# Kernel optimization log

Measured on AMD Instinct MI355X. Metric: run time of the kernel, lower is better.

Reference implementation:

```python
import jax, jax.numpy as jnp
import numpy as np
from functools import partial

B, N = 4, 4096
WIDTH, HEADS, HD = 768, 12, 64
MINI, CONV_W = 16, 4
TTT_BASE_LR = 1.0
THETA = 10000.0
EPS = 1e-6


def _rope_table():
    half = HD // 2
    freqs = 1.0 / THETA ** (np.arange(0, HD, 2)[:half].astype(np.float32) / HD)
    t = np.arange(2 * MINI)
    f = np.outer(t, freqs).astype(np.float32)
    return jnp.asarray(np.cos(f)), jnp.asarray(np.sin(f))

_COS, _SIN = _rope_table()


def apply_rope(x, cos, sin):
    # x: [B,N,H,HD]; cos/sin: [N, HD//2]; pairs are (x[2i], x[2i+1])
    xe, xo = x[..., 0::2], x[..., 1::2]
    c, s = cos[None, :, None, :], sin[None, :, None, :]
    return jnp.stack([xe * c - xo * s, xe * s + xo * c], axis=-1).reshape(x.shape)


def ln_fwd(x, g, b):
    mu = x.mean(-1, keepdims=True)
    std = jnp.sqrt(x.var(-1, keepdims=True) + EPS)
    return g * ((x - mu) / std) + b


def ln_fused_l2_bwd(x, target, g, b):
    # grad of 0.5*||LN(x)-target||^2 w.r.t. x (official TTT fused form)
    D = x.shape[-1]
    mu = x.mean(-1, keepdims=True)
    std = jnp.sqrt(x.var(-1, keepdims=True) + EPS)
    x_hat = (x - mu) / std
    gxh = ((g * x_hat + b) - target) * g
    return (D * gxh - gxh.sum(-1, keepdims=True)
            - x_hat * (gxh * x_hat).sum(-1, keepdims=True)) / (D * std)


def causal_dwconv(x, kernel, bias):
    # depthwise causal conv: x [B,N,C], kernel [W,1,C], left-pad W-1
    y = jax.lax.conv_general_dilated(
        x, kernel, (1,), [(CONV_W - 1, 0)],
        dimension_numbers=('NWC', 'WIO', 'NWC'), feature_group_count=WIDTH)
    return y + bias


def _mini_step(ln_g, ln_b, carry, inp):
    W1, b1h = carry
    XQ, XK, XV, eta = inp  # [m,hd] x3, eta [m,m]
    Z1 = XK @ W1 + b1h
    grad = ln_fused_l2_bwd(Z1, XV - XK, ln_g, ln_b)
    Attn = jnp.tril(XQ @ XK.T)
    b1_bar = b1h - jnp.tril(eta) @ grad
    Z1_bar = XQ @ W1 - (eta * Attn) @ grad + b1_bar
    last_eta = eta[-1][:, None]
    W1_new = W1 - (last_eta * XK).T @ grad
    b1_new = b1h - jnp.sum(last_eta * grad, axis=0, keepdims=True)
    out = XQ + ln_fwd(Z1_bar, ln_g, ln_b)
    return (W1_new, b1_new), out


def ttt_forward(hidden_states, wq, wv, wo, wg,
                conv_q_kernel, conv_q_bias, conv_k_kernel, conv_k_bias,
                W1, b1, ttt_norm_scale, ttt_norm_bias,
                lr_kernel, lr_bias, learnable_token_idx,
                post_norm_scale, post_norm_bias):
    Bsz, Nlen, _ = hidden_states.shape
    xqk = hidden_states @ wq
    XV = hidden_states @ wv
    XQ = causal_dwconv(xqk, conv_q_kernel, conv_q_bias)
    XK = causal_dwconv(xqk, conv_k_kernel, conv_k_bias)
    XQ = XQ.reshape(Bsz, Nlen, HEADS, HD)
    XK = XK.reshape(Bsz, Nlen, HEADS, HD)
    XV = XV.reshape(Bsz, Nlen, HEADS, HD)

    pos = jnp.arange(Nlen) % MINI  # RoPE restarts each mini-batch (official)
    XQ = apply_rope(XQ, _COS[pos], _SIN[pos])
    XK = apply_rope(XK, _COS[pos], _SIN[pos])

    def to_mb(x):  # [B,N,H,hd] -> [B,H,n_mini,mini,hd]
        return x.reshape(Bsz, -1, MINI, HEADS, HD).transpose(0, 3, 1, 2, 4)
    XQ, XK, XV = to_mb(XQ), to_mb(XK), to_mb(XV)

    # learnable per-head, per-token learning rate -> eta [B,H,n_mini,mini,mini]
    X_mb = hidden_states.reshape(Bsz, -1, MINI, WIDTH)
    ttt_lr = jax.nn.sigmoid(jnp.einsum('bnmw,hw->bhnm', X_mb, lr_kernel[..., 0])
                            + lr_bias[None, :, None, :])
    ttt_lr = TTT_BASE_LR * ttt_lr / HD
    token_idx = jnp.maximum(1.0 / jnp.arange(1, MINI + 1, dtype=jnp.float32)
                            + learnable_token_idx, 0.0)
    eta = token_idx[None, None, None, :, None] * ttt_lr[:, :, :, None, :]

    def per_head(xq, xk, xv, e, w1, b1h, g, bln):
        step = partial(_mini_step, g, bln)
        _, out = jax.lax.scan(step, (w1, b1h), (xq, xk, xv, e))
        return out.reshape(-1, HD)  # [N, hd]

    per_batch = jax.vmap(per_head, in_axes=(0, 0, 0, 0, 0, 0, 0, 0))
    out = jax.vmap(per_batch, in_axes=(0, 0, 0, 0, None, None, None, None))(
        XQ, XK, XV, eta, W1, b1, ttt_norm_scale, ttt_norm_bias)  # [B,H,N,hd]
    out = out.transpose(0, 2, 1, 3).reshape(Bsz, Nlen, WIDTH)

    z = ln_fwd(out, post_norm_scale, post_norm_bias)  # post_norm
    gate = jax.nn.gelu(hidden_states @ wg)            # GLU gating
    return (gate * z) @ wo


def setup_inputs() -> dict:
    key = jax.random.key(0)
    ks = jax.random.split(key, 12)
    std = 0.02
    f32 = jnp.float32
    return {
        'hidden_states': jax.random.normal(ks[0], (B, N, WIDTH), f32),
        'wq': jax.random.normal(ks[1], (WIDTH, HEADS * HD), f32) * std,
        'wv': jax.random.normal(ks[2], (WIDTH, HEADS * HD), f32) * std,
        'wo': jax.random.normal(ks[3], (WIDTH, WIDTH), f32) * std,
        'wg': jax.random.normal(ks[4], (WIDTH, WIDTH), f32) * std,
        'conv_q_kernel': jax.random.normal(ks[5], (CONV_W, 1, WIDTH), f32) * 0.5,
        'conv_q_bias': jnp.zeros((WIDTH,), f32),
        'conv_k_kernel': jax.random.normal(ks[6], (CONV_W, 1, WIDTH), f32) * 0.5,
        'conv_k_bias': jnp.zeros((WIDTH,), f32),
        'W1': jax.random.normal(ks[7], (HEADS, HD, HD), f32) * std,
        'b1': jnp.zeros((HEADS, 1, HD), f32),
        'ttt_norm_scale': jnp.ones((HEADS, HD), f32),
        'ttt_norm_bias': jnp.zeros((HEADS, HD), f32),
        'lr_kernel': jax.random.normal(ks[8], (HEADS, WIDTH, 1), f32) * std,
        'lr_bias': jnp.zeros((HEADS, 1), f32),
        'learnable_token_idx': jax.random.normal(ks[9], (MINI,), f32) * 0.01,
        'post_norm_scale': jnp.ones((WIDTH,), f32),
        'post_norm_bias': jnp.zeros((WIDTH,), f32),
    }


def reference(hidden_states, wq, wv, wo, wg, conv_q_kernel, conv_q_bias,
              conv_k_kernel, conv_k_bias, W1, b1, ttt_norm_scale, ttt_norm_bias,
              lr_kernel, lr_bias, learnable_token_idx, post_norm_scale, post_norm_bias):
    return ttt_forward(hidden_states, wq, wv, wo, wg, conv_q_kernel, conv_q_bias,
                       conv_k_kernel, conv_k_bias, W1, b1, ttt_norm_scale,
                       ttt_norm_bias, lr_kernel, lr_bias, learnable_token_idx,
                       post_norm_scale, post_norm_bias)
```

## Files before the change

### kernel.cpp

```cpp
#include <hip/hip_runtime.h>
#include <math.h>

#define WIDTH 768
#define HEADS 12
#define HD 64
#define MINI 16
#define NSEQ 4096
#define BATCH 4
#define NMB (NSEQ/MINI)
#define EPS 1e-6f

typedef __attribute__((ext_vector_type(8))) short bf16x8;
typedef __attribute__((ext_vector_type(4))) float f32x4;
typedef __attribute__((ext_vector_type(4))) int   i32x4;

__device__ __forceinline__ float bfu2f(unsigned short h) {
    return __uint_as_float(((unsigned)h) << 16);
}
__device__ __forceinline__ void tsplit(float f, unsigned short& h, unsigned short& l) {
    unsigned uh = __float_as_uint(f) & 0xffff0000u;
    h = (unsigned short)(uh >> 16);
    l = (unsigned short)(__float_as_uint(f - __uint_as_float(uh)) >> 16);
}
__device__ __forceinline__ unsigned tpack(float f) {
    unsigned uh = __float_as_uint(f) & 0xffff0000u;
    return uh | (__float_as_uint(f - __uint_as_float(uh)) >> 16);
}
__device__ __forceinline__ void barrier_lgkm() {
    asm volatile("s_waitcnt lgkmcnt(0)\n\ts_barrier" ::: "memory");
}

__global__ __launch_bounds__(256)
void hsplit_kernel(const float* __restrict__ in, unsigned short* __restrict__ hi,
                   unsigned short* __restrict__ lo)
{
    size_t idx = ((size_t)blockIdx.x * 256 + threadIdx.x) * 4;
    float4 v = *(const float4*)(in + idx);
    ushort4 h, l;
    tsplit(v.x, h.x, l.x); tsplit(v.y, h.y, l.y);
    tsplit(v.z, h.z, l.z); tsplit(v.w, h.w, l.w);
    *(ushort4*)(hi + idx) = h;
    *(ushort4*)(lo + idx) = l;
}

__global__ __launch_bounds__(256)
void wtconv_kernel(const float* __restrict__ w, unsigned short* __restrict__ hiT,
                   unsigned short* __restrict__ loT)
{
    __shared__ float sT[64][65];
    int k0 = blockIdx.y * 64, n0 = blockIdx.x * 64;
    int t = threadIdx.x, r = t >> 2, cs = (t & 3) * 16;
#pragma unroll
    for (int i = 0; i < 16; i += 4)
        *(float4*)&sT[r][cs + i] = *(const float4*)&w[(size_t)(k0 + r) * WIDTH + n0 + cs + i];
    __syncthreads();
    ushort4 hb[4], lb[4];
#pragma unroll
    for (int i = 0; i < 16; i++) {
        unsigned short hh, ll;
        tsplit(sT[cs + i][r], hh, ll);
        ((unsigned short*)hb)[i] = hh;
        ((unsigned short*)lb)[i] = ll;
    }
#pragma unroll
    for (int i = 0; i < 4; i++) {
        *(ushort4*)&hiT[(size_t)(n0 + r) * WIDTH + k0 + cs + i * 4] = hb[i];
        *(ushort4*)&loT[(size_t)(n0 + r) * WIDTH + k0 + cs + i * 4] = lb[i];
    }
}

template<int ACT>
__global__ __launch_bounds__(256, 2)
void gemm_bf3(const unsigned short* __restrict__ Ah, const unsigned short* __restrict__ Al,
              const unsigned short* __restrict__ BhT, const unsigned short* __restrict__ BlT,
              float* __restrict__ C, int M, int N, int K)
{
    __shared__ unsigned short sAh[128 * 40], sAl[128 * 40];
    __shared__ unsigned short sBh[128 * 40], sBl[128 * 40];
    const int tid = threadIdx.x;
    const int bm = blockIdx.y * 128, bn = blockIdx.x * 128;
    const int w = tid >> 6, lane = tid & 63, quad = lane >> 4, m16 = lane & 15;
    const int mw = (w & 1) * 64, nw = (w >> 1) * 64;
    const int srow = tid >> 1, sseg = (tid & 1) * 16;
    f32x4 acc[4][4];
#pragma unroll
    for (int a = 0; a < 4; a++)
#pragma unroll
        for (int c = 0; c < 4; c++) acc[a][c] = (f32x4){0.f, 0.f, 0.f, 0.f};

    for (int k0 = 0; k0 < K; k0 += 32) {
        uint4 va0 = *(const uint4*)(Ah + (size_t)(bm + srow) * K + k0 + sseg);
        uint4 va1 = *(const uint4*)(Ah + (size_t)(bm + srow) * K + k0 + sseg + 8);
        uint4 vb0 = *(const uint4*)(Al + (size_t)(bm + srow) * K + k0 + sseg);
        uint4 vb1 = *(const uint4*)(Al + (size_t)(bm + srow) * K + k0 + sseg + 8);
        uint4 vc0 = *(const uint4*)(BhT + (size_t)(bn + srow) * K + k0 + sseg);
        uint4 vc1 = *(const uint4*)(BhT + (size_t)(bn + srow) * K + k0 + sseg + 8);
        uint4 vd0 = *(const uint4*)(BlT + (size_t)(bn + srow) * K + k0 + sseg);
        uint4 vd1 = *(const uint4*)(BlT + (size_t)(bn + srow) * K + k0 + sseg + 8);
        __syncthreads();
        *(uint4*)&sAh[srow * 40 + sseg] = va0; *(uint4*)&sAh[srow * 40 + sseg + 8] = va1;
        *(uint4*)&sAl[srow * 40 + sseg] = vb0; *(uint4*)&sAl[srow * 40 + sseg + 8] = vb1;
        *(uint4*)&sBh[srow * 40 + sseg] = vc0; *(uint4*)&sBh[srow * 40 + sseg + 8] = vc1;
        *(uint4*)&sBl[srow * 40 + sseg] = vd0; *(uint4*)&sBl[srow * 40 + sseg + 8] = vd1;
        __syncthreads();
        bf16x8 ah[4], al[4];
#pragma unroll
        for (int mt = 0; mt < 4; mt++) {
            ah[mt] = *(const bf16x8*)&sAh[(mw + mt * 16 + m16) * 40 + quad * 8];
            al[mt] = *(const bf16x8*)&sAl[(mw + mt * 16 + m16) * 40 + quad * 8];
        }
#pragma unroll
        for (int nt = 0; nt < 4; nt++) {
            bf16x8 bh8 = *(const bf16x8*)&sBh[(nw + nt * 16 + m16) * 40 + quad * 8];
            bf16x8 bl8 = *(const bf16x8*)&sBl[(nw + nt * 16 + m16) * 40 + quad * 8];
#pragma unroll
            for (int mt = 0; mt < 4; mt++) {
                acc[mt][nt] = __builtin_amdgcn_mfma_f32_16x16x32_bf16(ah[mt], bh8, acc[mt][nt], 0, 0, 0);
                acc[mt][nt] = __builtin_amdgcn_mfma_f32_16x16x32_bf16(al[mt], bh8, acc[mt][nt], 0, 0, 0);
                acc[mt][nt] = __builtin_amdgcn_mfma_f32_16x16x32_bf16(ah[mt], bl8, acc[mt][nt], 0, 0, 0);
            }
        }
    }
#pragma unroll
    for (int mt = 0; mt < 4; mt++)
#pragma unroll
        for (int nt = 0; nt < 4; nt++)
#pragma unroll
            for (int r = 0; r < 4; r++) {
                float v = acc[mt][nt][r];
                if (ACT == 1) {
                    float inner = 0.7978845608028654f * (v + 0.044715f * v * v * v);
                    v = 0.5f * v * (1.0f + tanhf(inner));
                }
                C[(size_t)(bm + mw + mt * 16 + quad * 4 + r) * N + bn + nw + nt * 16 + m16] = v;
            }
}

__global__ __launch_bounds__(384)
void conv_rope_kernel(const float* __restrict__ xqk,
                      const float* __restrict__ kq, const float* __restrict__ bq,
                      const float* __restrict__ kk, const float* __restrict__ bk,
                      unsigned short* __restrict__ XQh, unsigned short* __restrict__ XQl,
                      unsigned short* __restrict__ XKh, unsigned short* __restrict__ XKl)
{
    int bid = blockIdx.x;
    int n = bid & (NSEQ - 1);
    int b = bid >> 12;
    int p = threadIdx.x;
    int c = p * 2;
    int pp = p & 31;
    float qe = bq[c], qo = bq[c + 1], ke = bk[c], ko = bk[c + 1];
#pragma unroll
    for (int w = 0; w < 4; w++) {
        int nn = n - 3 + w;
        if (nn >= 0) {
            const float* xr = xqk + ((size_t)(bid - n + nn)) * WIDTH + c;
            float xe = xr[0], xo = xr[1];
            qe = fmaf(xe, kq[w * WIDTH + c], qe);
            qo = fmaf(xo, kq[w * WIDTH + c + 1], qo);
            ke = fmaf(xe, kk[w * WIDTH + c], ke);
            ko = fmaf(xo, kk[w * WIDTH + c + 1], ko);
        }
    }
    int pos = n & (MINI - 1);
    float freq = expf(-(float)pp * (9.210340371976184f / 32.0f));
    float ang = (float)pos * freq;
    float c_ = cosf(ang), s_ = sinf(ang);
    int hh = p >> 5;
    int cc = pp * 2;
    size_t o = ((size_t)(b * HEADS + hh) * NSEQ + n) * 64 + cc;
    float q0 = qe * c_ - qo * s_, q1 = qe * s_ + qo * c_;
    float k0 = ke * c_ - ko * s_, k1 = ke * s_ + ko * c_;
    ushort2 h2, l2;
    tsplit(q0, h2.x, l2.x); tsplit(q1, h2.y, l2.y);
    *(ushort2*)&XQh[o] = h2; *(ushort2*)&XQl[o] = l2;
    tsplit(k0, h2.x, l2.x); tsplit(k1, h2.y, l2.y);
    *(ushort2*)&XKh[o] = h2; *(ushort2*)&XKl[o] = l2;
}

__global__ __launch_bounds__(256)
void lr_kernel(const float* __restrict__ hidden, const float* __restrict__ lrk,
               const float* __restrict__ lrb, float* __restrict__ lr_buf)
{
    int wave = threadIdx.x >> 6;
    int lane = threadIdx.x & 63;
    int row = blockIdx.x * 4 + wave;
    int b = row >> 12;
    int n = row & (NSEQ - 1);
    const float* hr = hidden + (size_t)row * WIDTH;
    float hv[12];
#pragma unroll
    for (int t = 0; t < 12; t++) hv[t] = hr[lane + 64 * t];
    for (int h = 0; h < HEADS; h++) {
        const float* lk = lrk + h * WIDTH;
        float acc = 0.f;
#pragma unroll
        for (int t = 0; t < 12; t++) acc = fmaf(hv[t], lk[lane + 64 * t], acc);
#pragma unroll
        for (int m = 1; m < 64; m <<= 1) acc += __shfl_xor(acc, m);
        if (lane == 0) {
            float s = 1.0f / (1.0f + __expf(-(acc + lrb[h])));
            lr_buf[((size_t)(b * HEADS + h)) * NSEQ + n] = s * (1.0f / HD);
        }
    }
}

__global__ __launch_bounds__(256)
void scan3_kernel(const unsigned short* __restrict__ XQh, const unsigned short* __restrict__ XQl,
                  const unsigned short* __restrict__ XKh, const unsigned short* __restrict__ XKl,
                  const float* __restrict__ XVb, const float* __restrict__ lr_buf,
                  const float* __restrict__ W1g, const float* __restrict__ b1g,
                  const float* __restrict__ gln, const float* __restrict__ blnv,
                  const float* __restrict__ lti, float* __restrict__ out)
{
    __shared__ unsigned sXKp[16 * 68];
    __shared__ unsigned sGE[16 * 68];
    __shared__ unsigned sCB[16 * 20];
    __shared__ float    sU[64 * 68];
    __shared__ float    sRed1[16 * 12], sRed2[16 * 12], sRed3[16 * 12];
    __shared__ float    sB1d[64];

    const int tid = threadIdx.x;
    const int w = tid >> 6, lane = tid & 63;
    const int quad = lane >> 4, m16 = lane & 15;
    const int bh = blockIdx.x, b = bh / HEADS, h = bh - b * HEADS;
    const int jc = 16 * w + m16;
    const int j4 = 16 * w + quad * 4;

    float g4[4], b4[4], b1v[4];
#pragma unroll
    for (int r = 0; r < 4; r++) {
        g4[r] = gln[h * 64 + j4 + r];
        b4[r] = blnv[h * 64 + j4 + r];
        b1v[r] = b1g[h * 64 + j4 + r];
    }
    const float tok15 = fmaxf(1.0f / 16.0f + lti[15], 0.0f);
    float tki[4];
#pragma unroll
    for (int r = 0; r < 4; r++)
        tki[r] = fmaxf(1.0f / (float)(quad * 4 + r + 1) + lti[quad * 4 + r], 0.0f) / tok15;

    float W1f[2][8]; bf16x8 w1h[2], w1l[2];
#pragma unroll
    for (int kt = 0; kt < 2; kt++)
#pragma unroll
        for (int e = 0; e < 8; e++) {
            float f = W1g[h * 4096 + (kt * 32 + quad * 8 + e) * 64 + jc];
            W1f[kt][e] = f;
            unsigned short hh, ll; tsplit(f, hh, ll);
            w1h[kt][e] = (short)hh; w1l[kt][e] = (short)ll;
        }

    const unsigned short* xqh = XQh + (size_t)bh * NSEQ * 64;
    const unsigned short* xql = XQl + (size_t)bh * NSEQ * 64;
    const unsigned short* xkh = XKh + (size_t)bh * NSEQ * 64;
    const unsigned short* xkl = XKl + (size_t)bh * NSEQ * 64;
    const float* xvB = XVb + (size_t)b * NSEQ * WIDTH + h * 64;
    const float* lrB = lr_buf + (size_t)bh * NSEQ;
    float* outB = out + (size_t)b * NSEQ * WIDTH + h * 64;

    bf16x8 ones8;
#pragma unroll
    for (int e = 0; e < 8; e++) ones8[e] = (short)0x3F80;
    const bf16x8 zf = {0, 0, 0, 0, 0, 0, 0, 0};

    bf16x8 pqh[2], pql[2], pkh[2], pkl[2];
    float4 pxv; ushort4 pth, ptl, poh, pol; float plr;
    {
        const size_t tok = m16;
#pragma unroll
        for (int kt = 0; kt < 2; kt++) {
            pqh[kt] = *(const bf16x8*)(xqh + tok * 64 + kt * 32 + quad * 8);
            pql[kt] = *(const bf16x8*)(xql + tok * 64 + kt * 32 + quad * 8);
            pkh[kt] = *(const bf16x8*)(xkh + tok * 64 + kt * 32 + quad * 8);
            pkl[kt] = *(const bf16x8*)(xkl + tok * 64 + kt * 32 + quad * 8);
        }
        pxv = *(const float4*)(xvB + tok * WIDTH + j4);
        pth = *(const ushort4*)(xkh + tok * 64 + j4);
        ptl = *(const ushort4*)(xkl + tok * 64 + j4);
        poh = *(const ushort4*)(xqh + tok * 64 + j4);
        pol = *(const ushort4*)(xql + tok * 64 + j4);
        plr = lrB[m16];
    }

    for (int s = 0; s < NMB; s++) {
        bf16x8 qh[2] = {pqh[0], pqh[1]}, ql[2] = {pql[0], pql[1]};
        bf16x8 kh[2] = {pkh[0], pkh[1]}, kl[2] = {pkl[0], pkl[1]};
        float xv4[4] = {pxv.x, pxv.y, pxv.z, pxv.w};
        float xkt4[4], xqo4[4];
        xkt4[0] = bfu2f(pth.x) + bfu2f(ptl.x); xkt4[1] = bfu2f(pth.y) + bfu2f(ptl.y);
        xkt4[2] = bfu2f(pth.z) + bfu2f(ptl.z); xkt4[3] = bfu2f(pth.w) + bfu2f(ptl.w);
        xqo4[0] = bfu2f(poh.x) + bfu2f(pol.x); xqo4[1] = bfu2f(poh.y) + bfu2f(pol.y);
        xqo4[2] = bfu2f(poh.z) + bfu2f(pol.z); xqo4[3] = bfu2f(poh.w) + bfu2f(pol.w);
        const float lrc = plr;
        const float sc = tok15 * lrc;

#pragma unroll
        for (int kt = 0; kt < 2; kt++) {
            i32x4 p0, p1;
#pragma unroll
            for (int e = 0; e < 4; e++)
                p0[e] = (int)((((unsigned)(unsigned short)kh[kt][e]) << 16) | (unsigned short)kl[kt][e]);
#pragma unroll
            for (int e = 0; e < 4; e++)
                p1[e] = (int)((((unsigned)(unsigned short)kh[kt][4 + e]) << 16) | (unsigned short)kl[kt][4 + e]);
            *(i32x4*)&sXKp[m16 * 68 + kt * 32 + quad * 8] = p0;
            *(i32x4*)&sXKp[m16 * 68 + kt * 32 + quad * 8 + 4] = p1;
        }

        {
            const int sn = (s + 1 < NMB) ? s + 1 : s;
            const size_t tok = (size_t)sn * 16 + m16;
#pragma unroll
            for (int kt = 0; kt < 2; kt++) {
                pqh[kt] = *(const bf16x8*)(xqh + tok * 64 + kt * 32 + quad * 8);
                pql[kt] = *(const bf16x8*)(xql + tok * 64 + kt * 32 + quad * 8);
                pkh[kt] = *(const bf16x8*)(xkh + tok * 64 + kt * 32 + quad * 8);
                pkl[kt] = *(const bf16x8*)(xkl + tok * 64 + kt * 32 + quad * 8);
            }
            pxv = *(const float4*)(xvB + tok * WIDTH + j4);
            pth = *(const ushort4*)(xkh + tok * 64 + j4);
            ptl = *(const ushort4*)(xkl + tok * 64 + j4);
            poh = *(const ushort4*)(xqh + tok * 64 + j4);
            pol = *(const ushort4*)(xql + tok * 64 + j4);
            plr = lrB[(size_t)sn * 16 + m16];
        }

        f32x4 z1 = {0.f, 0.f, 0.f, 0.f}, zq = {0.f, 0.f, 0.f, 0.f};
#pragma unroll
        for (int kt = 0; kt < 2; kt++) {
            z1 = __builtin_amdgcn_mfma_f32_16x16x32_bf16(w1h[kt], kh[kt], z1, 0, 0, 0);
            z1 = __builtin_amdgcn_mfma_f32_16x16x32_bf16(w1h[kt], kl[kt], z1, 0, 0, 0);
            z1 = __builtin_amdgcn_mfma_f32_16x16x32_bf16(w1l[kt], kh[kt], z1, 0, 0, 0);
            zq = __builtin_amdgcn_mfma_f32_16x16x32_bf16(w1h[kt], qh[kt], zq, 0, 0, 0);
            zq = __builtin_amdgcn_mfma_f32_16x16x32_bf16(w1h[kt], ql[kt], zq, 0, 0, 0);
            zq = __builtin_amdgcn_mfma_f32_16x16x32_bf16(w1l[kt], qh[kt], zq, 0, 0, 0);
        }
        f32x4 at = {0.f, 0.f, 0.f, 0.f};
        if (w == 0) {
#pragma unroll
            for (int kt = 0; kt < 2; kt++) {
                at = __builtin_amdgcn_mfma_f32_16x16x32_bf16(qh[kt], kh[kt], at, 0, 0, 0);
                at = __builtin_amdgcn_mfma_f32_16x16x32_bf16(qh[kt], kl[kt], at, 0, 0, 0);
                at = __builtin_amdgcn_mfma_f32_16x16x32_bf16(ql[kt], kh[kt], at, 0, 0, 0);
            }
        }
#pragma unroll
        for (int r = 0; r < 4; r++) z1[r] += b1v[r];

        float s1p = (z1[0] + z1[1]) + (z1[2] + z1[3]);
        float s2p = (z1[0] * z1[0] + z1[1] * z1[1]) + (z1[2] * z1[2] + z1[3] * z1[3]);
        s1p += __shfl_xor(s1p, 16); s2p += __shfl_xor(s2p, 16);
        s1p += __shfl_xor(s1p, 32); s2p += __shfl_xor(s2p, 32);
        if (quad == 0) *(float2*)&sRed1[m16 * 12 + 2 * w] = make_float2(s1p, s2p);
        if (w == 0) {
            i32x4 cw;
#pragma unroll
            for (int r = 0; r < 4; r++) {
                float v = (m16 <= quad * 4 + r) ? -(tki[r] * (1.0f + at[r])) : 0.0f;
                cw[r] = (int)tpack(v);
            }
            *(i32x4*)&sCB[m16 * 20 + quad * 4] = cw;
        }
        barrier_lgkm();

        float4 ra = *(const float4*)&sRed1[m16 * 12];
        float4 rb = *(const float4*)&sRed1[m16 * 12 + 4];
        float S1 = ra.x + ra.z + rb.x + rb.z;
        float S2 = ra.y + ra.w + rb.y + rb.w;
        float mu = S1 * (1.0f / 64.0f);
        float var = S2 * (1.0f / 64.0f) - mu * mu;
        float rstd = rsqrtf(var + EPS);
        float xh[4], gxh[4];
#pragma unroll
        for (int r = 0; r < 4; r++) {
            xh[r] = (z1[r] - mu) * rstd;
            gxh[r] = fmaf(g4[r], xh[r], b4[r] - (xv4[r] - xkt4[r])) * g4[r];
        }
        float t1p = (gxh[0] + gxh[1]) + (gxh[2] + gxh[3]);
        float t2p = (gxh[0] * xh[0] + gxh[1] * xh[1]) + (gxh[2] * xh[2] + gxh[3] * xh[3]);
        t1p += __shfl_xor(t1p, 16); t2p += __shfl_xor(t2p, 16);
        t1p += __shfl_xor(t1p, 32); t2p += __shfl_xor(t2p, 32);
        if (quad == 0) *(float2*)&sRed2[m16 * 12 + 2 * w] = make_float2(t1p, t2p);
        barrier_lgkm();

        ra = *(const float4*)&sRed2[m16 * 12];
        rb = *(const float4*)&sRed2[m16 * 12 + 4];
        float T1 = ra.x + ra.z + rb.x + rb.z;
        float T2 = ra.y + ra.w + rb.y + rb.w;
        i32x4 gw;
#pragma unroll
        for (int r = 0; r < 4; r++) {
            float grad = (64.0f * gxh[r] - T1 - xh[r] * T2) * (rstd * (1.0f / 64.0f));
            gw[r] = (int)tpack(sc * grad);
        }
        *(i32x4*)&sGE[m16 * 68 + j4] = gw;
        barrier_lgkm();

        bf16x8 akh8 = zf, akl8 = zf;
#pragma unroll
        for (int e = 0; e < 8; e++) {
            unsigned u = (quad < 2) ? sXKp[(quad * 8 + e) * 68 + 16 * w + m16] : 0u;
            akh8[e] = (short)(u >> 16); akl8[e] = (short)(u & 0xffffu);
        }
        bf16x8 agh = zf, agl = zf;
#pragma unroll
        for (int nt = 0; nt < 4; nt++) {
            bf16x8 gh8 = zf, gl8 = zf;
#pragma unroll
            for (int e = 0; e < 8; e++) {
                unsigned u = (quad < 2) ? sGE[(quad * 8 + e) * 68 + 16 * nt + m16] : 0u;
                gh8[e] = (short)(u >> 16); gl8[e] = (short)(u & 0xffffu);
            }
            if (nt == w) { agh = gh8; agl = gl8; }
            f32x4 ua = {0.f, 0.f, 0.f, 0.f};
            ua = __builtin_amdgcn_mfma_f32_16x16x32_bf16(akh8, gh8, ua, 0, 0, 0);
            ua = __builtin_amdgcn_mfma_f32_16x16x32_bf16(akl8, gh8, ua, 0, 0, 0);
            ua = __builtin_amdgcn_mfma_f32_16x16x32_bf16(akh8, gl8, ua, 0, 0, 0);
#pragma unroll
            for (int r = 0; r < 4; r++)
                sU[(16 * w + quad * 4 + r) * 68 + 16 * nt + m16] = ua[r];
            if (w == 1) {
                f32x4 bda = {0.f, 0.f, 0.f, 0.f};
                bda = __builtin_amdgcn_mfma_f32_16x16x32_bf16(ones8, gh8, bda, 0, 0, 0);
                bda = __builtin_amdgcn_mfma_f32_16x16x32_bf16(ones8, gl8, bda, 0, 0, 0);
                if (quad == 0) sB1d[16 * nt + m16] = bda[0];
            }
        }
        bf16x8 cbh = zf, cbl = zf;
#pragma unroll
        for (int e = 0; e < 8; e++) {
            unsigned u = (quad < 2) ? sCB[(quad * 8 + e) * 20 + m16] : 0u;
            cbh[e] = (short)(u >> 16); cbl[e] = (short)(u & 0xffffu);
        }
        zq = __builtin_amdgcn_mfma_f32_16x16x32_bf16(agh, cbh, zq, 0, 0, 0);
        zq = __builtin_amdgcn_mfma_f32_16x16x32_bf16(agl, cbh, zq, 0, 0, 0);
        zq = __builtin_amdgcn_mfma_f32_16x16x32_bf16(agh, cbl, zq, 0, 0, 0);
        float zb[4];
#pragma unroll
        for (int r = 0; r < 4; r++) zb[r] = zq[r] + b1v[r];
        float u1p = (zb[0] + zb[1]) + (zb[2] + zb[3]);
        float u2p = (zb[0] * zb[0] + zb[1] * zb[1]) + (zb[2] * zb[2] + zb[3] * zb[3]);
        u1p += __shfl_xor(u1p, 16); u2p += __shfl_xor(u2p, 16);
        u1p += __shfl_xor(u1p, 32); u2p += __shfl_xor(u2p, 32);
        if (quad == 0) *(float2*)&sRed3[m16 * 12 + 2 * w] = make_float2(u1p, u2p);
        barrier_lgkm();

        ra = *(const float4*)&sRed3[m16 * 12];
        rb = *(const float4*)&sRed3[m16 * 12 + 4];
        float V1 = ra.x + ra.z + rb.x + rb.z;
        float V2 = ra.y + ra.w + rb.y + rb.w;
        float mu2 = V1 * (1.0f / 64.0f);
        float va2 = V2 * (1.0f / 64.0f) - mu2 * mu2;
        float rs2 = rsqrtf(va2 + EPS);
        float4 ov;
        ov.x = xqo4[0] + fmaf(g4[0], (zb[0] - mu2) * rs2, b4[0]);
        ov.y = xqo4[1] + fmaf(g4[1], (zb[1] - mu2) * rs2, b4[1]);
        ov.z = xqo4[2] + fmaf(g4[2], (zb[2] - mu2) * rs2, b4[2]);
        ov.w = xqo4[3] + fmaf(g4[3], (zb[3] - mu2) * rs2, b4[3]);
        *(float4*)&outB[(size_t)(s * 16 + m16) * WIDTH + j4] = ov;

#pragma unroll
        for (int kt = 0; kt < 2; kt++)
#pragma unroll
            for (int e = 0; e < 8; e++) {
                float f = W1f[kt][e] - sU[(kt * 32 + quad * 8 + e) * 68 + jc];
                W1f[kt][e] = f;
                unsigned short hh, ll; tsplit(f, hh, ll);
                w1h[kt][e] = (short)hh; w1l[kt][e] = (short)ll;
            }
        float4 bdv = *(const float4*)&sB1d[j4];
        b1v[0] -= bdv.x; b1v[1] -= bdv.y; b1v[2] -= bdv.z; b1v[3] -= bdv.w;
    }
}

__global__ __launch_bounds__(256)
void postgate_kernel(const float* __restrict__ tout, const float* __restrict__ gate,
                     const float* __restrict__ ps, const float* __restrict__ pb,
                     unsigned short* __restrict__ gzh, unsigned short* __restrict__ gzl)
{
    __shared__ float red[8];
    int row = blockIdx.x;
    int tid = threadIdx.x;
    const float* x = tout + (size_t)row * WIDTH;
    float v[3];
    float s1 = 0, s2 = 0;
#pragma unroll
    for (int t = 0; t < 3; t++) { v[t] = x[tid + 256 * t]; s1 += v[t]; s2 += v[t] * v[t]; }
#pragma unroll
    for (int m = 1; m < 64; m <<= 1) { s1 += __shfl_xor(s1, m); s2 += __shfl_xor(s2, m); }
    int wave = tid >> 6, lane = tid & 63;
    if (lane == 0) { red[wave] = s1; red[4 + wave] = s2; }
    __syncthreads();
    s1 = red[0] + red[1] + red[2] + red[3];
    s2 = red[4] + red[5] + red[6] + red[7];
    float mu = s1 * (1.0f / WIDTH);
    float var = s2 * (1.0f / WIDTH) - mu * mu;
    float rstd = rsqrtf(var + EPS);
#pragma unroll
    for (int t = 0; t < 3; t++) {
        int c = tid + 256 * t;
        float z = ps[c] * (v[t] - mu) * rstd + pb[c];
        float gv = gate[(size_t)row * WIDTH + c] * z;
        unsigned short hh, ll; tsplit(gv, hh, ll);
        gzh[(size_t)row * WIDTH + c] = hh;
        gzl[(size_t)row * WIDTH + c] = ll;
    }
}

extern "C" void kernel_launch(void* const* d_in, const int* in_sizes, int n_in,
                              void* d_out, int out_size, void* d_ws, size_t ws_size,
                              hipStream_t stream)
{
    (void)in_sizes; (void)n_in; (void)out_size; (void)ws_size;
    const float* hidden = (const float*)d_in[0];
    const float* wq  = (const float*)d_in[1];
    const float* wv  = (const float*)d_in[2];
    const float* wo  = (const float*)d_in[3];
    const float* wg  = (const float*)d_in[4];
    const float* ckq = (const float*)d_in[5];
    const float* cbq = (const float*)d_in[6];
    const float* ckk = (const float*)d_in[7];
    const float* cbk = (const float*)d_in[8];
    const float* W1  = (const float*)d_in[9];
    const float* b1  = (const float*)d_in[10];
    const float* tns = (const float*)d_in[11];
    const float* tnb = (const float*)d_in[12];
    const float* lrk = (const float*)d_in[13];
    const float* lrb = (const float*)d_in[14];
    const float* lti = (const float*)d_in[15];
    const float* pns = (const float*)d_in[16];
    const float* pnb = (const float*)d_in[17];
    float* out = (float*)d_out;

    const size_t BIG = (size_t)BATCH * NSEQ * WIDTH;
    float* ws  = (float*)d_ws;
    float* ws0 = ws;
    float* ws1 = ws + BIG;
    float* ws2 = ws + 2 * BIG;
    float* ws3 = ws + 3 * BIG;
    float* lrbuf = ws + 4 * BIG;

    unsigned short* wqThi = (unsigned short*)ws2;
    unsigned short* wqTlo = wqThi + WIDTH * WIDTH;
    unsigned short* wvThi = wqTlo + WIDTH * WIDTH;
    unsigned short* wvTlo = wvThi + WIDTH * WIDTH;
    unsigned short* wgThi = wvTlo + WIDTH * WIDTH;
    unsigned short* wgTlo = wgThi + WIDTH * WIDTH;

    unsigned short* Ahi = (unsigned short*)ws3;
    unsigned short* Alo = Ahi + BIG;

    unsigned short* XQhi = (unsigned short*)ws2;
    unsigned short* XQlo = XQhi + BIG;
    unsigned short* XKhi = (unsigned short*)ws3;
    unsigned short* XKlo = XKhi + BIG;

    unsigned short* woThi = (unsigned short*)ws1;
    unsigned short* woTlo = woThi + WIDTH * WIDTH;
    unsigned short* gzhi  = (unsigned short*)ws2;
    unsigned short* gzlo  = gzhi + BIG;

    float* xqk  = ws0;
    float* XVb  = ws1;
    float* gate = out;
    float* ttto = ws0;

    int M = BATCH * NSEQ;
    dim3 gg(WIDTH / 128, M / 128);
    dim3 wtg(WIDTH / 64, WIDTH / 64);

    hsplit_kernel<<<(unsigned)(BIG / 1024), 256, 0, stream>>>(hidden, Ahi, Alo);
    wtconv_kernel<<<wtg, 256, 0, stream>>>(wq, wqThi, wqTlo);
    wtconv_kernel<<<wtg, 256, 0, stream>>>(wv, wvThi, wvTlo);
    wtconv_kernel<<<wtg, 256, 0, stream>>>(wg, wgThi, wgTlo);
    gemm_bf3<0><<<gg, 256, 0, stream>>>(Ahi, Alo, wqThi, wqTlo, xqk, M, WIDTH, WIDTH);
    gemm_bf3<0><<<gg, 256, 0, stream>>>(Ahi, Alo, wvThi, wvTlo, XVb, M, WIDTH, WIDTH);
    gemm_bf3<1><<<gg, 256, 0, stream>>>(Ahi, Alo, wgThi, wgTlo, gate, M, WIDTH, WIDTH);
    conv_rope_kernel<<<M, 384, 0, stream>>>(xqk, ckq, cbq, ckk, cbk, XQhi, XQlo, XKhi, XKlo);
    lr_kernel<<<M / 4, 256, 0, stream>>>(hidden, lrk, lrb, lrbuf);
    scan3_kernel<<<BATCH * HEADS, 256, 0, stream>>>(XQhi, XQlo, XKhi, XKlo, XVb, lrbuf,
                                                    W1, b1, tns, tnb, lti, ttto);
    wtconv_kernel<<<wtg, 256, 0, stream>>>(wo, woThi, woTlo);
    postgate_kernel<<<M, 256, 0, stream>>>(ttto, gate, pns, pnb, gzhi, gzlo);
    gemm_bf3<0><<<gg, 256, 0, stream>>>(gzhi, gzlo, woThi, woTlo, out, M, WIDTH, WIDTH);
}
```

Measured before the change: 1.335 ms.

## Fuse scan with gate GEMM in a persistent mega-kernel and split A inline

Replaces the separate hsplit pass by splitting fp32 activations into hi/lo bf16 inside the GEMM load, and batches the three weight conversions into one launch. The 48-block sequential scan now runs in a 960-block mega kernel alongside the gate GEMM and wo conversion, so the otherwise idle CUs do useful work during the latency-bound scan. The scan also merges its LayerNorm-backward reductions into one barrier stage. This adds shared-memory unions and workload dispatch complexity, and the mega kernel's 40 KB shared footprint may limit occupancy.

```diff
diff --git a/kernel.cpp b/kernel.cpp
--- a/kernel.cpp
+++ b/kernel.cpp
@@ -30,35 +30,36 @@
     asm volatile("s_waitcnt lgkmcnt(0)\n\ts_barrier" ::: "memory");
 }
 
-__global__ __launch_bounds__(256)
-void hsplit_kernel(const float* __restrict__ in, unsigned short* __restrict__ hi,
-                   unsigned short* __restrict__ lo)
-{
-    size_t idx = ((size_t)blockIdx.x * 256 + threadIdx.x) * 4;
-    float4 v = *(const float4*)(in + idx);
-    ushort4 h, l;
-    tsplit(v.x, h.x, l.x); tsplit(v.y, h.y, l.y);
-    tsplit(v.z, h.z, l.z); tsplit(v.w, h.w, l.w);
-    *(ushort4*)(hi + idx) = h;
-    *(ushort4*)(lo + idx) = l;
-}
-
-__global__ __launch_bounds__(256)
-void wtconv_kernel(const float* __restrict__ w, unsigned short* __restrict__ hiT,
-                   unsigned short* __restrict__ loT)
-{
-    __shared__ float sT[64][65];
-    int k0 = blockIdx.y * 64, n0 = blockIdx.x * 64;
+struct ScanSM {
+    unsigned sXKp[16 * 68];
+    unsigned sGE[16 * 68];
+    unsigned sCB[16 * 20];
+    float    sU[64 * 68];
+    float    sRedM[16 * 36];
+    float    sRed3[16 * 36];
+    float    sB1d[64];
+};
+struct GemmSM {
+    unsigned short sAh[128 * 40], sAl[128 * 40];
+    unsigned short sBh[128 * 40], sBl[128 * 40];
+};
+struct WtSM { float sT[64][65]; };
+#define SMEM_BYTES 40960
+
+__device__ void wtconv_body(char* smraw, int n0, int k0, const float* __restrict__ w,
+                            unsigned short* __restrict__ hiT, unsigned short* __restrict__ loT)
+{
+    WtSM* W = (WtSM*)smraw;
     int t = threadIdx.x, r = t >> 2, cs = (t & 3) * 16;
 #pragma unroll
     for (int i = 0; i < 16; i += 4)
-        *(float4*)&sT[r][cs + i] = *(const float4*)&w[(size_t)(k0 + r) * WIDTH + n0 + cs + i];
+        *(float4*)&W->sT[r][cs + i] = *(const float4*)&w[(size_t)(k0 + r) * WIDTH + n0 + cs + i];
     __syncthreads();
     ushort4 hb[4], lb[4];
 #pragma unroll
     for (int i = 0; i < 16; i++) {
         unsigned short hh, ll;
-        tsplit(sT[cs + i][r], hh, ll);
+        tsplit(W->sT[cs + i][r], hh, ll);
         ((unsigned short*)hb)[i] = hh;
         ((unsigned short*)lb)[i] = ll;
     }
@@ -69,16 +70,18 @@
     }
 }
 
-template<int ACT>
-__global__ __launch_bounds__(256, 2)
-void gemm_bf3(const unsigned short* __restrict__ Ah, const unsigned short* __restrict__ Al,
-              const unsigned short* __restrict__ BhT, const unsigned short* __restrict__ BlT,
-              float* __restrict__ C, int M, int N, int K)
-{
-    __shared__ unsigned short sAh[128 * 40], sAl[128 * 40];
-    __shared__ unsigned short sBh[128 * 40], sBl[128 * 40];
+template<int ACT, int SPLITA>
+__device__ void gemm_body(char* smraw, int by,
+                          const float* __restrict__ Af,
+                          const unsigned short* __restrict__ APh,
+                          const unsigned short* __restrict__ APl,
+                          const unsigned short* __restrict__ BhT,
+                          const unsigned short* __restrict__ BlT,
+                          float* __restrict__ C, int ldc, int K)
+{
+    GemmSM* g = (GemmSM*)smraw;
     const int tid = threadIdx.x;
-    const int bm = blockIdx.y * 128, bn = blockIdx.x * 128;
+    const int bm = by * 128;
     const int w = tid >> 6, lane = tid & 63, quad = lane >> 4, m16 = lane & 15;
     const int mw = (w & 1) * 64, nw = (w >> 1) * 64;
     const int srow = tid >> 1, sseg = (tid & 1) * 16;
@@ -89,30 +92,48 @@
         for (int c = 0; c < 4; c++) acc[a][c] = (f32x4){0.f, 0.f, 0.f, 0.f};
 
     for (int k0 = 0; k0 < K; k0 += 32) {
-        uint4 va0 = *(const uint4*)(Ah + (size_t)(bm + srow) * K + k0 + sseg);
-        uint4 va1 = *(const uint4*)(Ah + (size_t)(bm + srow) * K + k0 + sseg + 8);
-        uint4 vb0 = *(const uint4*)(Al + (size_t)(bm + srow) * K + k0 + sseg);
-        uint4 vb1 = *(const uint4*)(Al + (size_t)(bm + srow) * K + k0 + sseg + 8);
-        uint4 vc0 = *(const uint4*)(BhT + (size_t)(bn + srow) * K + k0 + sseg);
-        uint4 vc1 = *(const uint4*)(BhT + (size_t)(bn + srow) * K + k0 + sseg + 8);
-        uint4 vd0 = *(const uint4*)(BlT + (size_t)(bn + srow) * K + k0 + sseg);
-        uint4 vd1 = *(const uint4*)(BlT + (size_t)(bn + srow) * K + k0 + sseg + 8);
-        __syncthreads();
-        *(uint4*)&sAh[srow * 40 + sseg] = va0; *(uint4*)&sAh[srow * 40 + sseg + 8] = va1;
-        *(uint4*)&sAl[srow * 40 + sseg] = vb0; *(uint4*)&sAl[srow * 40 + sseg + 8] = vb1;
-        *(uint4*)&sBh[srow * 40 + sseg] = vc0; *(uint4*)&sBh[srow * 40 + sseg + 8] = vc1;
-        *(uint4*)&sBl[srow * 40 + sseg] = vd0; *(uint4*)&sBl[srow * 40 + sseg + 8] = vd1;
+        uint4 vb0 = *(const uint4*)(BhT + (size_t)srow * K + k0 + sseg);
+        uint4 vb1 = *(const uint4*)(BhT + (size_t)srow * K + k0 + sseg + 8);
+        uint4 vd0 = *(const uint4*)(BlT + (size_t)srow * K + k0 + sseg);
+        uint4 vd1 = *(const uint4*)(BlT + (size_t)srow * K + k0 + sseg + 8);
+        if (SPLITA) {
+            const float* Ap = Af + (size_t)(bm + srow) * K + k0 + sseg;
+            float4 f0 = *(const float4*)(Ap);
+            float4 f1 = *(const float4*)(Ap + 4);
+            float4 f2 = *(const float4*)(Ap + 8);
+            float4 f3 = *(const float4*)(Ap + 12);
+            __syncthreads();
+            unsigned short hs[16], ls[16];
+            float fv[16] = {f0.x, f0.y, f0.z, f0.w, f1.x, f1.y, f1.z, f1.w,
+                            f2.x, f2.y, f2.z, f2.w, f3.x, f3.y, f3.z, f3.w};
+#pragma unroll
+            for (int i = 0; i < 16; i++) tsplit(fv[i], hs[i], ls[i]);
+            *(uint4*)&g->sAh[srow * 40 + sseg]     = *(uint4*)&hs[0];
+            *(uint4*)&g->sAh[srow * 40 + sseg + 8] = *(uint4*)&hs[8];
+            *(uint4*)&g->sAl[srow * 40 + sseg]     = *(uint4*)&ls[0];
+            *(uint4*)&g->sAl[srow * 40 + sseg + 8] = *(uint4*)&ls[8];
+        } else {
+            uint4 va0 = *(const uint4*)(APh + (size_t)(bm + srow) * K + k0 + sseg);
+            uint4 va1 = *(const uint4*)(APh + (size_t)(bm + srow) * K + k0 + sseg + 8);
+            uint4 vc0 = *(const uint4*)(APl + (size_t)(bm + srow) * K + k0 + sseg);
+            uint4 vc1 = *(const uint4*)(APl + (size_t)(bm + srow) * K + k0 + sseg + 8);
+            __syncthreads();
+            *(uint4*)&g->sAh[srow * 40 + sseg] = va0; *(uint4*)&g->sAh[srow * 40 + sseg + 8] = va1;
+            *(uint4*)&g->sAl[srow * 40 + sseg] = vc0; *(uint4*)&g->sAl[srow * 40 + sseg + 8] = vc1;
+        }
+        *(uint4*)&g->sBh[srow * 40 + sseg] = vb0; *(uint4*)&g->sBh[srow * 40 + sseg + 8] = vb1;
+        *(uint4*)&g->sBl[srow * 40 + sseg] = vd0; *(uint4*)&g->sBl[srow * 40 + sseg + 8] = vd1;
         __syncthreads();
         bf16x8 ah[4], al[4];
 #pragma unroll
         for (int mt = 0; mt < 4; mt++) {
-            ah[mt] = *(const bf16x8*)&sAh[(mw + mt * 16 + m16) * 40 + quad * 8];
-            al[mt] = *(const bf16x8*)&sAl[(mw + mt * 16 + m16) * 40 + quad * 8];
+            ah[mt] = *(const bf16x8*)&g->sAh[(mw + mt * 16 + m16) * 40 + quad * 8];
+            al[mt] = *(const bf16x8*)&g->sAl[(mw + mt * 16 + m16) * 40 + quad * 8];
         }
 #pragma unroll
         for (int nt = 0; nt < 4; nt++) {
-            bf16x8 bh8 = *(const bf16x8*)&sBh[(nw + nt * 16 + m16) * 40 + quad * 8];
-            bf16x8 bl8 = *(const bf16x8*)&sBl[(nw + nt * 16 + m16) * 40 + quad * 8];
+            bf16x8 bh8 = *(const bf16x8*)&g->sBh[(nw + nt * 16 + m16) * 40 + quad * 8];
+            bf16x8 bl8 = *(const bf16x8*)&g->sBl[(nw + nt * 16 + m16) * 40 + quad * 8];
 #pragma unroll
             for (int mt = 0; mt < 4; mt++) {
                 acc[mt][nt] = __builtin_amdgcn_mfma_f32_16x16x32_bf16(ah[mt], bh8, acc[mt][nt], 0, 0, 0);
@@ -132,8 +153,353 @@
                     float inner = 0.7978845608028654f * (v + 0.044715f * v * v * v);
                     v = 0.5f * v * (1.0f + tanhf(inner));
                 }
-                C[(size_t)(bm + mw + mt * 16 + quad * 4 + r) * N + bn + nw + nt * 16 + m16] = v;
-            }
+                C[(size_t)(bm + mw + mt * 16 + quad * 4 + r) * ldc + nw + nt * 16 + m16] = v;
+            }
+}
+
+__device__ void scan_body(char* smraw, int bh,
+    const unsigned short* __restrict__ XQh, const unsigned short* __restrict__ XQl,
+    const unsigned short* __restrict__ XKh, const unsigned short* __restrict__ XKl,
+    const float* __restrict__ XVb, const float* __restrict__ lr_buf,
+    const float* __restrict__ W1g, const float* __restrict__ b1g,
+    const float* __restrict__ gln, const float* __restrict__ blnv,
+    const float* __restrict__ lti, float* __restrict__ out)
+{
+    ScanSM* S = (ScanSM*)smraw;
+    const int tid = threadIdx.x;
+    const int w = tid >> 6, lane = tid & 63;
+    const int quad = lane >> 4, m16 = lane & 15;
+    const int b = bh / HEADS, h = bh - b * HEADS;
+    const int jc = 16 * w + m16;
+    const int j4 = 16 * w + quad * 4;
+
+    float g4[4], b4[4], b1v[4], gg4[4];
+#pragma unroll
+    for (int r = 0; r < 4; r++) {
+        g4[r] = gln[h * 64 + j4 + r];
+        b4[r] = blnv[h * 64 + j4 + r];
+        b1v[r] = b1g[h * 64 + j4 + r];
+        gg4[r] = g4[r] * g4[r];
+    }
+    const float tok15 = fmaxf(1.0f / 16.0f + lti[15], 0.0f);
+    float tki[4];
+#pragma unroll
+    for (int r = 0; r < 4; r++)
+        tki[r] = fmaxf(1.0f / (float)(quad * 4 + r + 1) + lti[quad * 4 + r], 0.0f) / tok15;
+
+    float ags = (gg4[0] + gg4[1]) + (gg4[2] + gg4[3]);
+    ags += __shfl_xor(ags, 16); ags += __shfl_xor(ags, 32);
+    if (lane == 0) S->sB1d[w] = ags;
+    __syncthreads();
+    const float Ag2 = S->sB1d[0] + S->sB1d[1] + S->sB1d[2] + S->sB1d[3];
+
+    float W1f[2][8]; bf16x8 w1h[2], w1l[2];
+#pragma unroll
+    for (int kt = 0; kt < 2; kt++)
+#pragma unroll
+        for (int e = 0; e < 8; e++) {
+            float f = W1g[h * 4096 + (kt * 32 + quad * 8 + e) * 64 + jc];
+            W1f[kt][e] = f;
+            unsigned short hh, ll; tsplit(f, hh, ll);
+            w1h[kt][e] = (short)hh; w1l[kt][e] = (short)ll;
+        }
+
+    const unsigned short* xqh = XQh + (size_t)bh * NSEQ * 64;
+    const unsigned short* xql = XQl + (size_t)bh * NSEQ * 64;
+    const unsigned short* xkh = XKh + (size_t)bh * NSEQ * 64;
+    const unsigned short* xkl = XKl + (size_t)bh * NSEQ * 64;
+    const float* xvB = XVb + (size_t)b * NSEQ * WIDTH + h * 64;
+    const float* lrB = lr_buf + (size_t)bh * NSEQ;
+    float* outB = out + (size_t)b * NSEQ * WIDTH + h * 64;
+
+    bf16x8 ones8;
+#pragma unroll
+    for (int e = 0; e < 8; e++) ones8[e] = (short)0x3F80;
+    const bf16x8 zf = {0, 0, 0, 0, 0, 0, 0, 0};
+
+    bf16x8 pqh[2], pql[2], pkh[2], pkl[2];
+    float4 pxv; ushort4 pth, ptl, poh, pol; float plr;
+    {
+        const size_t tok = m16;
+#pragma unroll
+        for (int kt = 0; kt < 2; kt++) {
+            pqh[kt] = *(const bf16x8*)(xqh + tok * 64 + kt * 32 + quad * 8);
+            pql[kt] = *(const bf16x8*)(xql + tok * 64 + kt * 32 + quad * 8);
+            pkh[kt] = *(const bf16x8*)(xkh + tok * 64 + kt * 32 + quad * 8);
+            pkl[kt] = *(const bf16x8*)(xkl + tok * 64 + kt * 32 + quad * 8);
+        }
+        pxv = *(const float4*)(xvB + tok * WIDTH + j4);
+        pth = *(const ushort4*)(xkh + tok * 64 + j4);
+        ptl = *(const ushort4*)(xkl + tok * 64 + j4);
+        poh = *(const ushort4*)(xqh + tok * 64 + j4);
+        pol = *(const ushort4*)(xql + tok * 64 + j4);
+        plr = lrB[m16];
+    }
+
+    for (int s = 0; s < NMB; s++) {
+        bf16x8 qh[2] = {pqh[0], pqh[1]}, ql[2] = {pql[0], pql[1]};
+        bf16x8 kh[2] = {pkh[0], pkh[1]}, kl[2] = {pkl[0], pkl[1]};
+        float xv4[4] = {pxv.x, pxv.y, pxv.z, pxv.w};
+        float xkt4[4], xqo4[4];
+        xkt4[0] = bfu2f(pth.x) + bfu2f(ptl.x); xkt4[1] = bfu2f(pth.y) + bfu2f(ptl.y);
+        xkt4[2] = bfu2f(pth.z) + bfu2f(ptl.z); xkt4[3] = bfu2f(pth.w) + bfu2f(ptl.w);
+        xqo4[0] = bfu2f(poh.x) + bfu2f(pol.x); xqo4[1] = bfu2f(poh.y) + bfu2f(pol.y);
+        xqo4[2] = bfu2f(poh.z) + bfu2f(pol.z); xqo4[3] = bfu2f(poh.w) + bfu2f(pol.w);
+        const float lrc = plr;
+        const float sc = tok15 * lrc;
+
+#pragma unroll
+        for (int kt = 0; kt < 2; kt++) {
+            i32x4 p0, p1;
+#pragma unroll
+            for (int e = 0; e < 4; e++)
+                p0[e] = (int)((((unsigned)(unsigned short)kh[kt][e]) << 16) | (unsigned short)kl[kt][e]);
+#pragma unroll
+            for (int e = 0; e < 4; e++)
+                p1[e] = (int)((((unsigned)(unsigned short)kh[kt][4 + e]) << 16) | (unsigned short)kl[kt][4 + e]);
+            *(i32x4*)&S->sXKp[m16 * 68 + kt * 32 + quad * 8] = p0;
+            *(i32x4*)&S->sXKp[m16 * 68 + kt * 32 + quad * 8 + 4] = p1;
+        }
+
+        {
+            const int sn = (s + 1 < NMB) ? s + 1 : s;
+            const size_t tok = (size_t)sn * 16 + m16;
+#pragma unroll
+            for (int kt = 0; kt < 2; kt++) {
+                pqh[kt] = *(const bf16x8*)(xqh + tok * 64 + kt * 32 + quad * 8);
+                pql[kt] = *(const bf16x8*)(xql + tok * 64 + kt * 32 + quad * 8);
+                pkh[kt] = *(const bf16x8*)(xkh + tok * 64 + kt * 32 + quad * 8);
+                pkl[kt] = *(const bf16x8*)(xkl + tok * 64 + kt * 32 + quad * 8);
+            }
+            pxv = *(const float4*)(xvB + tok * WIDTH + j4);
+            pth = *(const ushort4*)(xkh + tok * 64 + j4);
+            ptl = *(const ushort4*)(xkl + tok * 64 + j4);
+            poh = *(const ushort4*)(xqh + tok * 64 + j4);
+            pol = *(const ushort4*)(xql + tok * 64 + j4);
+            plr = lrB[(size_t)sn * 16 + m16];
+        }
+
+        f32x4 z1 = {0.f, 0.f, 0.f, 0.f}, zq = {0.f, 0.f, 0.f, 0.f};
+#pragma unroll
+        for (int kt = 0; kt < 2; kt++) {
+            z1 = __builtin_amdgcn_mfma_f32_16x16x32_bf16(w1h[kt], kh[kt], z1, 0, 0, 0);
+            z1 = __builtin_amdgcn_mfma_f32_16x16x32_bf16(w1h[kt], kl[kt], z1, 0, 0, 0);
+            z1 = __builtin_amdgcn_mfma_f32_16x16x32_bf16(w1l[kt], kh[kt], z1, 0, 0, 0);
+            zq = __builtin_amdgcn_mfma_f32_16x16x32_bf16(w1h[kt], qh[kt], zq, 0, 0, 0);
+            zq = __builtin_amdgcn_mfma_f32_16x16x32_bf16(w1h[kt], ql[kt], zq, 0, 0, 0);
+            zq = __builtin_amdgcn_mfma_f32_16x16x32_bf16(w1l[kt], qh[kt], zq, 0, 0, 0);
+        }
+        f32x4 at = {0.f, 0.f, 0.f, 0.f};
+        if (w == 3) {
+#pragma unroll
+            for (int kt = 0; kt < 2; kt++) {
+                at = __builtin_amdgcn_mfma_f32_16x16x32_bf16(qh[kt], kh[kt], at, 0, 0, 0);
+                at = __builtin_amdgcn_mfma_f32_16x16x32_bf16(qh[kt], kl[kt], at, 0, 0, 0);
+                at = __builtin_amdgcn_mfma_f32_16x16x32_bf16(ql[kt], kh[kt], at, 0, 0, 0);
+            }
+        }
+#pragma unroll
+        for (int r = 0; r < 4; r++) z1[r] += b1v[r];
+
+        float c1g[4];
+        float s1 = 0.f, s2 = 0.f, a1 = 0.f, a4 = 0.f, a3 = 0.f, a5 = 0.f;
+#pragma unroll
+        for (int r = 0; r < 4; r++) {
+            float z = z1[r];
+            float t = xv4[r] - xkt4[r];
+            c1g[r] = (b4[r] - t) * g4[r];
+            s1 += z; s2 += z * z;
+            float gz = gg4[r] * z;
+            a1 += gz; a4 += gz * z;
+            a3 += c1g[r]; a5 += c1g[r] * z;
+        }
+        s1 += __shfl_xor(s1, 16); s2 += __shfl_xor(s2, 16);
+        a1 += __shfl_xor(a1, 16); a4 += __shfl_xor(a4, 16);
+        a3 += __shfl_xor(a3, 16); a5 += __shfl_xor(a5, 16);
+        s1 += __shfl_xor(s1, 32); s2 += __shfl_xor(s2, 32);
+        a1 += __shfl_xor(a1, 32); a4 += __shfl_xor(a4, 32);
+        a3 += __shfl_xor(a3, 32); a5 += __shfl_xor(a5, 32);
+        if (quad == 0) {
+            *(float4*)&S->sRedM[m16 * 36 + w * 8]     = make_float4(s1, s2, a1, a4);
+            *(float4*)&S->sRedM[m16 * 36 + w * 8 + 4] = make_float4(a3, a5, 0.f, 0.f);
+        }
+        if (w == 3) {
+            i32x4 cw;
+#pragma unroll
+            for (int r = 0; r < 4; r++) {
+                float v = (m16 <= quad * 4 + r) ? -(tki[r] * (1.0f + at[r])) : 0.0f;
+                cw[r] = (int)tpack(v);
+            }
+            *(i32x4*)&S->sCB[m16 * 20 + quad * 4] = cw;
+        }
+        barrier_lgkm();
+
+        float S1 = 0.f, S2 = 0.f, A1 = 0.f, A4 = 0.f, A3 = 0.f, A5 = 0.f;
+#pragma unroll
+        for (int w2 = 0; w2 < 4; w2++) {
+            float4 pa = *(const float4*)&S->sRedM[m16 * 36 + w2 * 8];
+            float4 pb = *(const float4*)&S->sRedM[m16 * 36 + w2 * 8 + 4];
+            S1 += pa.x; S2 += pa.y; A1 += pa.z; A4 += pa.w;
+            A3 += pb.x; A5 += pb.y;
+        }
+        float mu = S1 * (1.0f / 64.0f);
+        float var = S2 * (1.0f / 64.0f) - mu * mu;
+        float rstd = rsqrtf(var + EPS);
+        float T1 = rstd * (A1 - mu * Ag2) + A3;
+        float T2 = rstd * rstd * (A4 - 2.0f * mu * A1 + mu * mu * Ag2)
+                 + rstd * (A5 - mu * A3);
+        i32x4 gw;
+#pragma unroll
+        for (int r = 0; r < 4; r++) {
+            float xh = (z1[r] - mu) * rstd;
+            float gxh = gg4[r] * xh + c1g[r];
+            float grad = (64.0f * gxh - T1 - xh * T2) * (rstd * (1.0f / 64.0f));
+            gw[r] = (int)tpack(sc * grad);
+        }
+        *(i32x4*)&S->sGE[m16 * 68 + j4] = gw;
+        barrier_lgkm();
+
+        bf16x8 akh8 = zf, akl8 = zf;
+#pragma unroll
+        for (int e = 0; e < 8; e++) {
+            unsigned u = (quad < 2) ? S->sXKp[(quad * 8 + e) * 68 + 16 * w + m16] : 0u;
+            akh8[e] = (short)(u >> 16); akl8[e] = (short)(u & 0xffffu);
+        }
+        bf16x8 agh = zf, agl = zf;
+#pragma unroll
+        for (int nt = 0; nt < 4; nt++) {
+            bf16x8 gh8 = zf, gl8 = zf;
+#pragma unroll
+            for (int e = 0; e < 8; e++) {
+                unsigned u = (quad < 2) ? S->sGE[(quad * 8 + e) * 68 + 16 * nt + m16] : 0u;
+                gh8[e] = (short)(u >> 16); gl8[e] = (short)(u & 0xffffu);
+            }
+            if (nt == w) { agh = gh8; agl = gl8; }
+            f32x4 ua = {0.f, 0.f, 0.f, 0.f};
+            ua = __builtin_amdgcn_mfma_f32_16x16x32_bf16(akh8, gh8, ua, 0, 0, 0);
+            ua = __builtin_amdgcn_mfma_f32_16x16x32_bf16(akl8, gh8, ua, 0, 0, 0);
+            ua = __builtin_amdgcn_mfma_f32_16x16x32_bf16(akh8, gl8, ua, 0, 0, 0);
+#pragma unroll
+            for (int r = 0; r < 4; r++)
+                S->sU[(16 * w + quad * 4 + r) * 68 + 16 * nt + m16] = ua[r];
+            if (w == 1) {
+                f32x4 bda = {0.f, 0.f, 0.f, 0.f};
+                bda = __builtin_amdgcn_mfma_f32_16x16x32_bf16(ones8, gh8, bda, 0, 0, 0);
+                bda = __builtin_amdgcn_mfma_f32_16x16x32_bf16(ones8, gl8, bda, 0, 0, 0);
+                if (quad == 0) S->sB1d[16 * nt + m16] = bda[0];
+            }
+        }
+        bf16x8 cbh = zf, cbl = zf;
+#pragma unroll
+        for (int e = 0; e < 8; e++) {
+            unsigned u = (quad < 2) ? S->sCB[(quad * 8 + e) * 20 + m16] : 0u;
+            cbh[e] = (short)(u >> 16); cbl[e] = (short)(u & 0xffffu);
+        }
+        zq = __builtin_amdgcn_mfma_f32_16x16x32_bf16(agh, cbh, zq, 0, 0, 0);
+        zq = __builtin_amdgcn_mfma_f32_16x16x32_bf16(agl, cbh, zq, 0, 0, 0);
+        zq = __builtin_amdgcn_mfma_f32_16x16x32_bf16(agh, cbl, zq, 0, 0, 0);
+        float zb[4];
+#pragma unroll
+        for (int r = 0; r < 4; r++) zb[r] = zq[r] + b1v[r];
+        float u1p = (zb[0] + zb[1]) + (zb[2] + zb[3]);
+        float u2p = (zb[0] * zb[0] + zb[1] * zb[1]) + (zb[2] * zb[2] + zb[3] * zb[3]);
+        u1p += __shfl_xor(u1p, 16); u2p += __shfl_xor(u2p, 16);
+        u1p += __shfl_xor(u1p, 32); u2p += __shfl_xor(u2p, 32);
+        if (quad == 0) *(float2*)&S->sRed3[m16 * 36 + w * 8] = make_float2(u1p, u2p);
+        barrier_lgkm();
+
+        float V1 = 0.f, V2 = 0.f;
+#pragma unroll
+        for (int w2 = 0; w2 < 4; w2++) {
+            float2 p = *(const float2*)&S->sRed3[m16 * 36 + w2 * 8];
+            V1 += p.x; V2 += p.y;
+        }
+        float mu2 = V1 * (1.0f / 64.0f);
+        float va2 = V2 * (1.0f / 64.0f) - mu2 * mu2;
+        float rs2 = rsqrtf(va2 + EPS);
+        float4 ov;
+        ov.x = xqo4[0] + fmaf(g4[0], (zb[0] - mu2) * rs2, b4[0]);
+        ov.y = xqo4[1] + fmaf(g4[1], (zb[1] - mu2) * rs2, b4[1]);
+        ov.z = xqo4[2] + fmaf(g4[2], (zb[2] - mu2) * rs2, b4[2]);
+        ov.w = xqo4[3] + fmaf(g4[3], (zb[3] - mu2) * rs2, b4[3]);
+        *(float4*)&outB[(size_t)(s * 16 + m16) * WIDTH + j4] = ov;
+
+#pragma unroll
+        for (int kt = 0; kt < 2; kt++)
+#pragma unroll
+            for (int e = 0; e < 8; e++) {
+                float f = W1f[kt][e] - S->sU[(kt * 32 + quad * 8 + e) * 68 + jc];
+                W1f[kt][e] = f;
+                unsigned short hh, ll; tsplit(f, hh, ll);
+                w1h[kt][e] = (short)hh; w1l[kt][e] = (short)ll;
+            }
+        float4 bdv = *(const float4*)&S->sB1d[j4];
+        b1v[0] -= bdv.x; b1v[1] -= bdv.y; b1v[2] -= bdv.z; b1v[3] -= bdv.w;
+    }
+}
+
+__global__ __launch_bounds__(256, 2)
+void mega_kernel(const unsigned short* __restrict__ XQh, const unsigned short* __restrict__ XQl,
+                 const unsigned short* __restrict__ XKh, const unsigned short* __restrict__ XKl,
+                 const float* __restrict__ XVb, const float* __restrict__ lrbuf,
+                 const float* __restrict__ W1, const float* __restrict__ b1,
+                 const float* __restrict__ tns, const float* __restrict__ tnb,
+                 const float* __restrict__ lti, float* __restrict__ ttto,
+                 const float* __restrict__ wo, unsigned short* __restrict__ woThi,
+                 unsigned short* __restrict__ woTlo,
+                 const float* __restrict__ hidden, const unsigned short* __restrict__ wTgh,
+                 const unsigned short* __restrict__ wTgl, float* __restrict__ gate)
+{
+    __shared__ __align__(16) char sm[SMEM_BYTES];
+    int bid = blockIdx.x;
+    if (bid < 48) {
+        scan_body(sm, bid, XQh, XQl, XKh, XKl, XVb, lrbuf, W1, b1, tns, tnb, lti, ttto);
+    } else if (bid < 192) {
+        int idx = bid - 48;
+        wtconv_body(sm, (idx % 12) * 64, (idx / 12) * 64, wo, woThi, woTlo);
+    } else {
+        int idx = bid - 192;
+        int bx = idx % 6, by = idx / 6;
+        int bn = bx * 128;
+        gemm_body<1, 1>(sm, by, hidden, nullptr, nullptr,
+                        wTgh + (size_t)bn * WIDTH, wTgl + (size_t)bn * WIDTH,
+                        gate + bn, WIDTH, WIDTH);
+    }
+}
+
+__global__ __launch_bounds__(256, 2)
+void gemm_qv_kernel(const float* __restrict__ hidden,
+                    const unsigned short* __restrict__ wThi, const unsigned short* __restrict__ wTlo,
+                    float* __restrict__ xqk, float* __restrict__ XVb)
+{
+    __shared__ __align__(16) char sm[SMEM_BYTES];
+    int bn = blockIdx.x * 128;
+    float* C = (bn < WIDTH) ? (xqk + bn) : (XVb + bn - WIDTH);
+    gemm_body<0, 1>(sm, blockIdx.y, hidden, nullptr, nullptr,
+                    wThi + (size_t)bn * WIDTH, wTlo + (size_t)bn * WIDTH, C, WIDTH, WIDTH);
+}
+
+__global__ __launch_bounds__(256, 2)
+void gemm_out_kernel(const unsigned short* __restrict__ gzh, const unsigned short* __restrict__ gzl,
+                     const unsigned short* __restrict__ woThi, const unsigned short* __restrict__ woTlo,
+                     float* __restrict__ out)
+{
+    __shared__ __align__(16) char sm[SMEM_BYTES];
+    int bn = blockIdx.x * 128;
+    gemm_body<0, 0>(sm, blockIdx.y, nullptr, gzh, gzl,
+                    woThi + (size_t)bn * WIDTH, woTlo + (size_t)bn * WIDTH, out + bn, WIDTH, WIDTH);
+}
+
+__global__ __launch_bounds__(256)
+void wtconv3_kernel(const float* __restrict__ wq, const float* __restrict__ wv,
+                    const float* __restrict__ wg,
+                    unsigned short* __restrict__ hiT, unsigned short* __restrict__ loT)
+{
+    __shared__ __align__(16) char sm[sizeof(WtSM)];
+    int widx = blockIdx.z;
+    const float* src = (widx == 0) ? wq : ((widx == 1) ? wv : wg);
+    size_t off = (size_t)widx * WIDTH * WIDTH;
+    wtconv_body(sm, blockIdx.x * 64, blockIdx.y * 64, src, hiT + off, loT + off);
 }
 
 __global__ __launch_bounds__(384)
@@ -202,275 +568,6 @@
             float s = 1.0f / (1.0f + __expf(-(acc + lrb[h])));
             lr_buf[((size_t)(b * HEADS + h)) * NSEQ + n] = s * (1.0f / HD);
         }
-    }
-}
-
-__global__ __launch_bounds__(256)
-void scan3_kernel(const unsigned short* __restrict__ XQh, const unsigned short* __restrict__ XQl,
-                  const unsigned short* __restrict__ XKh, const unsigned short* __restrict__ XKl,
-                  const float* __restrict__ XVb, const float* __restrict__ lr_buf,
-                  const float* __restrict__ W1g, const float* __restrict__ b1g,
-                  const float* __restrict__ gln, const float* __restrict__ blnv,
-                  const float* __restrict__ lti, float* __restrict__ out)
-{
-    __shared__ unsigned sXKp[16 * 68];
-    __shared__ unsigned sGE[16 * 68];
-    __shared__ unsigned sCB[16 * 20];
-    __shared__ float    sU[64 * 68];
-    __shared__ float    sRed1[16 * 12], sRed2[16 * 12], sRed3[16 * 12];
-    __shared__ float    sB1d[64];
-
-    const int tid = threadIdx.x;
-    const int w = tid >> 6, lane = tid & 63;
-    const int quad = lane >> 4, m16 = lane & 15;
-    const int bh = blockIdx.x, b = bh / HEADS, h = bh - b * HEADS;
-    const int jc = 16 * w + m16;
-    const int j4 = 16 * w + quad * 4;
-
-    float g4[4], b4[4], b1v[4];
-#pragma unroll
-    for (int r = 0; r < 4; r++) {
-        g4[r] = gln[h * 64 + j4 + r];
-        b4[r] = blnv[h * 64 + j4 + r];
-        b1v[r] = b1g[h * 64 + j4 + r];
-    }
-    const float tok15 = fmaxf(1.0f / 16.0f + lti[15], 0.0f);
-    float tki[4];
-#pragma unroll
-    for (int r = 0; r < 4; r++)
-        tki[r] = fmaxf(1.0f / (float)(quad * 4 + r + 1) + lti[quad * 4 + r], 0.0f) / tok15;
-
-    float W1f[2][8]; bf16x8 w1h[2], w1l[2];
-#pragma unroll
-    for (int kt = 0; kt < 2; kt++)
-#pragma unroll
-        for (int e = 0; e < 8; e++) {
-            float f = W1g[h * 4096 + (kt * 32 + quad * 8 + e) * 64 + jc];
-            W1f[kt][e] = f;
-            unsigned short hh, ll; tsplit(f, hh, ll);
-            w1h[kt][e] = (short)hh; w1l[kt][e] = (short)ll;
-        }
-
-    const unsigned short* xqh = XQh + (size_t)bh * NSEQ * 64;
-    const unsigned short* xql = XQl + (size_t)bh * NSEQ * 64;
-    const unsigned short* xkh = XKh + (size_t)bh * NSEQ * 64;
-    const unsigned short* xkl = XKl + (size_t)bh * NSEQ * 64;
-    const float* xvB = XVb + (size_t)b * NSEQ * WIDTH + h * 64;
-    const float* lrB = lr_buf + (size_t)bh * NSEQ;
-    float* outB = out + (size_t)b * NSEQ * WIDTH + h * 64;
-
-    bf16x8 ones8;
-#pragma unroll
-    for (int e = 0; e < 8; e++) ones8[e] = (short)0x3F80;
-    const bf16x8 zf = {0, 0, 0, 0, 0, 0, 0, 0};
-
-    bf16x8 pqh[2], pql[2], pkh[2], pkl[2];
-    float4 pxv; ushort4 pth, ptl, poh, pol; float plr;
-    {
-        const size_t tok = m16;
-#pragma unroll
-        for (int kt = 0; kt < 2; kt++) {
-            pqh[kt] = *(const bf16x8*)(xqh + tok * 64 + kt * 32 + quad * 8);
-            pql[kt] = *(const bf16x8*)(xql + tok * 64 + kt * 32 + quad * 8);
-            pkh[kt] = *(const bf16x8*)(xkh + tok * 64 + kt * 32 + quad * 8);
-            pkl[kt] = *(const bf16x8*)(xkl + tok * 64 + kt * 32 + quad * 8);
-        }
-        pxv = *(const float4*)(xvB + tok * WIDTH + j4);
-        pth = *(const ushort4*)(xkh + tok * 64 + j4);
-        ptl = *(const ushort4*)(xkl + tok * 64 + j4);
-        poh = *(const ushort4*)(xqh + tok * 64 + j4);
-        pol = *(const ushort4*)(xql + tok * 64 + j4);
-        plr = lrB[m16];
-    }
-
-    for (int s = 0; s < NMB; s++) {
-        bf16x8 qh[2] = {pqh[0], pqh[1]}, ql[2] = {pql[0], pql[1]};
-        bf16x8 kh[2] = {pkh[0], pkh[1]}, kl[2] = {pkl[0], pkl[1]};
-        float xv4[4] = {pxv.x, pxv.y, pxv.z, pxv.w};
-        float xkt4[4], xqo4[4];
-        xkt4[0] = bfu2f(pth.x) + bfu2f(ptl.x); xkt4[1] = bfu2f(pth.y) + bfu2f(ptl.y);
-        xkt4[2] = bfu2f(pth.z) + bfu2f(ptl.z); xkt4[3] = bfu2f(pth.w) + bfu2f(ptl.w);
-        xqo4[0] = bfu2f(poh.x) + bfu2f(pol.x); xqo4[1] = bfu2f(poh.y) + bfu2f(pol.y);
-        xqo4[2] = bfu2f(poh.z) + bfu2f(pol.z); xqo4[3] = bfu2f(poh.w) + bfu2f(pol.w);
-        const float lrc = plr;
-        const float sc = tok15 * lrc;
-
-#pragma unroll
-        for (int kt = 0; kt < 2; kt++) {
-            i32x4 p0, p1;
-#pragma unroll
-            for (int e = 0; e < 4; e++)
-                p0[e] = (int)((((unsigned)(unsigned short)kh[kt][e]) << 16) | (unsigned short)kl[kt][e]);
-#pragma unroll
-            for (int e = 0; e < 4; e++)
-                p1[e] = (int)((((unsigned)(unsigned short)kh[kt][4 + e]) << 16) | (unsigned short)kl[kt][4 + e]);
-            *(i32x4*)&sXKp[m16 * 68 + kt * 32 + quad * 8] = p0;
-            *(i32x4*)&sXKp[m16 * 68 + kt * 32 + quad * 8 + 4] = p1;
-        }
-
-        {
-            const int sn = (s + 1 < NMB) ? s + 1 : s;
-            const size_t tok = (size_t)sn * 16 + m16;
-#pragma unroll
-            for (int kt = 0; kt < 2; kt++) {
-                pqh[kt] = *(const bf16x8*)(xqh + tok * 64 + kt * 32 + quad * 8);
-                pql[kt] = *(const bf16x8*)(xql + tok * 64 + kt * 32 + quad * 8);
-                pkh[kt] = *(const bf16x8*)(xkh + tok * 64 + kt * 32 + quad * 8);
-                pkl[kt] = *(const bf16x8*)(xkl + tok * 64 + kt * 32 + quad * 8);
-            }
-            pxv = *(const float4*)(xvB + tok * WIDTH + j4);
-            pth = *(const ushort4*)(xkh + tok * 64 + j4);
-            ptl = *(const ushort4*)(xkl + tok * 64 + j4);
-            poh = *(const ushort4*)(xqh + tok * 64 + j4);
-            pol = *(const ushort4*)(xql + tok * 64 + j4);
-            plr = lrB[(size_t)sn * 16 + m16];
-        }
-
-        f32x4 z1 = {0.f, 0.f, 0.f, 0.f}, zq = {0.f, 0.f, 0.f, 0.f};
-#pragma unroll
-        for (int kt = 0; kt < 2; kt++) {
-            z1 = __builtin_amdgcn_mfma_f32_16x16x32_bf16(w1h[kt], kh[kt], z1, 0, 0, 0);
-            z1 = __builtin_amdgcn_mfma_f32_16x16x32_bf16(w1h[kt], kl[kt], z1, 0, 0, 0);
-            z1 = __builtin_amdgcn_mfma_f32_16x16x32_bf16(w1l[kt], kh[kt], z1, 0, 0, 0);
-            zq = __builtin_amdgcn_mfma_f32_16x16x32_bf16(w1h[kt], qh[kt], zq, 0, 0, 0);
-            zq = __builtin_amdgcn_mfma_f32_16x16x32_bf16(w1h[kt], ql[kt], zq, 0, 0, 0);
-            zq = __builtin_amdgcn_mfma_f32_16x16x32_bf16(w1l[kt], qh[kt], zq, 0, 0, 0);
-        }
-        f32x4 at = {0.f, 0.f, 0.f, 0.f};
-        if (w == 0) {
-#pragma unroll
-            for (int kt = 0; kt < 2; kt++) {
-                at = __builtin_amdgcn_mfma_f32_16x16x32_bf16(qh[kt], kh[kt], at, 0, 0, 0);
-                at = __builtin_amdgcn_mfma_f32_16x16x32_bf16(qh[kt], kl[kt], at, 0, 0, 0);
-                at = __builtin_amdgcn_mfma_f32_16x16x32_bf16(ql[kt], kh[kt], at, 0, 0, 0);
-            }
-        }
-#pragma unroll
-        for (int r = 0; r < 4; r++) z1[r] += b1v[r];
-
-        float s1p = (z1[0] + z1[1]) + (z1[2] + z1[3]);
-        float s2p = (z1[0] * z1[0] + z1[1] * z1[1]) + (z1[2] * z1[2] + z1[3] * z1[3]);
-        s1p += __shfl_xor(s1p, 16); s2p += __shfl_xor(s2p, 16);
-        s1p += __shfl_xor(s1p, 32); s2p += __shfl_xor(s2p, 32);
-        if (quad == 0) *(float2*)&sRed1[m16 * 12 + 2 * w] = make_float2(s1p, s2p);
-        if (w == 0) {
-            i32x4 cw;
-#pragma unroll
-            for (int r = 0; r < 4; r++) {
-                float v = (m16 <= quad * 4 + r) ? -(tki[r] * (1.0f + at[r])) : 0.0f;
-                cw[r] = (int)tpack(v);
-            }
-            *(i32x4*)&sCB[m16 * 20 + quad * 4] = cw;
-        }
-        barrier_lgkm();
-
-        float4 ra = *(const float4*)&sRed1[m16 * 12];
-        float4 rb = *(const float4*)&sRed1[m16 * 12 + 4];
-        float S1 = ra.x + ra.z + rb.x + rb.z;
-        float S2 = ra.y + ra.w + rb.y + rb.w;
-        float mu = S1 * (1.0f / 64.0f);
-        float var = S2 * (1.0f / 64.0f) - mu * mu;
-        float rstd = rsqrtf(var + EPS);
-        float xh[4], gxh[4];
-#pragma unroll
-        for (int r = 0; r < 4; r++) {
-            xh[r] = (z1[r] - mu) * rstd;
-            gxh[r] = fmaf(g4[r], xh[r], b4[r] - (xv4[r] - xkt4[r])) * g4[r];
-        }
-        float t1p = (gxh[0] + gxh[1]) + (gxh[2] + gxh[3]);
-        float t2p = (gxh[0] * xh[0] + gxh[1] * xh[1]) + (gxh[2] * xh[2] + gxh[3] * xh[3]);
-        t1p += __shfl_xor(t1p, 16); t2p += __shfl_xor(t2p, 16);
-        t1p += __shfl_xor(t1p, 32); t2p += __shfl_xor(t2p, 32);
-        if (quad == 0) *(float2*)&sRed2[m16 * 12 + 2 * w] = make_float2(t1p, t2p);
-        barrier_lgkm();
-
-        ra = *(const float4*)&sRed2[m16 * 12];
-        rb = *(const float4*)&sRed2[m16 * 12 + 4];
-        float T1 = ra.x + ra.z + rb.x + rb.z;
-        float T2 = ra.y + ra.w + rb.y + rb.w;
-        i32x4 gw;
-#pragma unroll
-        for (int r = 0; r < 4; r++) {
-            float grad = (64.0f * gxh[r] - T1 - xh[r] * T2) * (rstd * (1.0f / 64.0f));
-            gw[r] = (int)tpack(sc * grad);
-        }
-        *(i32x4*)&sGE[m16 * 68 + j4] = gw;
-        barrier_lgkm();
-
-        bf16x8 akh8 = zf, akl8 = zf;
-#pragma unroll
-        for (int e = 0; e < 8; e++) {
-            unsigned u = (quad < 2) ? sXKp[(quad * 8 + e) * 68 + 16 * w + m16] : 0u;
-            akh8[e] = (short)(u >> 16); akl8[e] = (short)(u & 0xffffu);
-        }
-        bf16x8 agh = zf, agl = zf;
-#pragma unroll
-        for (int nt = 0; nt < 4; nt++) {
-            bf16x8 gh8 = zf, gl8 = zf;
-#pragma unroll
-            for (int e = 0; e < 8; e++) {
-                unsigned u = (quad < 2) ? sGE[(quad * 8 + e) * 68 + 16 * nt + m16] : 0u;
-                gh8[e] = (short)(u >> 16); gl8[e] = (short)(u & 0xffffu);
-            }
-            if (nt == w) { agh = gh8; agl = gl8; }
-            f32x4 ua = {0.f, 0.f, 0.f, 0.f};
-            ua = __builtin_amdgcn_mfma_f32_16x16x32_bf16(akh8, gh8, ua, 0, 0, 0);
-            ua = __builtin_amdgcn_mfma_f32_16x16x32_bf16(akl8, gh8, ua, 0, 0, 0);
-            ua = __builtin_amdgcn_mfma_f32_16x16x32_bf16(akh8, gl8, ua, 0, 0, 0);
-#pragma unroll
-            for (int r = 0; r < 4; r++)
-                sU[(16 * w + quad * 4 + r) * 68 + 16 * nt + m16] = ua[r];
-            if (w == 1) {
-                f32x4 bda = {0.f, 0.f, 0.f, 0.f};
-                bda = __builtin_amdgcn_mfma_f32_16x16x32_bf16(ones8, gh8, bda, 0, 0, 0);
-                bda = __builtin_amdgcn_mfma_f32_16x16x32_bf16(ones8, gl8, bda, 0, 0, 0);
-                if (quad == 0) sB1d[16 * nt + m16] = bda[0];
-            }
-        }
-        bf16x8 cbh = zf, cbl = zf;
-#pragma unroll
-        for (int e = 0; e < 8; e++) {
-            unsigned u = (quad < 2) ? sCB[(quad * 8 + e) * 20 + m16] : 0u;
-            cbh[e] = (short)(u >> 16); cbl[e] = (short)(u & 0xffffu);
-        }
-        zq = __builtin_amdgcn_mfma_f32_16x16x32_bf16(agh, cbh, zq, 0, 0, 0);
-        zq = __builtin_amdgcn_mfma_f32_16x16x32_bf16(agl, cbh, zq, 0, 0, 0);
-        zq = __builtin_amdgcn_mfma_f32_16x16x32_bf16(agh, cbl, zq, 0, 0, 0);
-        float zb[4];
-#pragma unroll
-        for (int r = 0; r < 4; r++) zb[r] = zq[r] + b1v[r];
-        float u1p = (zb[0] + zb[1]) + (zb[2] + zb[3]);
-        float u2p = (zb[0] * zb[0] + zb[1] * zb[1]) + (zb[2] * zb[2] + zb[3] * zb[3]);
-        u1p += __shfl_xor(u1p, 16); u2p += __shfl_xor(u2p, 16);
-        u1p += __shfl_xor(u1p, 32); u2p += __shfl_xor(u2p, 32);
-        if (quad == 0) *(float2*)&sRed3[m16 * 12 + 2 * w] = make_float2(u1p, u2p);
-        barrier_lgkm();
-
-        ra = *(const float4*)&sRed3[m16 * 12];
-        rb = *(const float4*)&sRed3[m16 * 12 + 4];
-        float V1 = ra.x + ra.z + rb.x + rb.z;
-        float V2 = ra.y + ra.w + rb.y + rb.w;
-        float mu2 = V1 * (1.0f / 64.0f);
-        float va2 = V2 * (1.0f / 64.0f) - mu2 * mu2;
-        float rs2 = rsqrtf(va2 + EPS);
-        float4 ov;
-        ov.x = xqo4[0] + fmaf(g4[0], (zb[0] - mu2) * rs2, b4[0]);
-        ov.y = xqo4[1] + fmaf(g4[1], (zb[1] - mu2) * rs2, b4[1]);
-        ov.z = xqo4[2] + fmaf(g4[2], (zb[2] - mu2) * rs2, b4[2]);
-        ov.w = xqo4[3] + fmaf(g4[3], (zb[3] - mu2) * rs2, b4[3]);
-        *(float4*)&outB[(size_t)(s * 16 + m16) * WIDTH + j4] = ov;
-
-#pragma unroll
-        for (int kt = 0; kt < 2; kt++)
-#pragma unroll
-            for (int e = 0; e < 8; e++) {
-                float f = W1f[kt][e] - sU[(kt * 32 + quad * 8 + e) * 68 + jc];
-                W1f[kt][e] = f;
-                unsigned short hh, ll; tsplit(f, hh, ll);
-                w1h[kt][e] = (short)hh; w1l[kt][e] = (short)ll;
-            }
-        float4 bdv = *(const float4*)&sB1d[j4];
-        b1v[0] -= bdv.x; b1v[1] -= bdv.y; b1v[2] -= bdv.z; b1v[3] -= bdv.w;
     }
 }
 
@@ -535,53 +632,33 @@
 
     const size_t BIG = (size_t)BATCH * NSEQ * WIDTH;
     float* ws  = (float*)d_ws;
-    float* ws0 = ws;
-    float* ws1 = ws + BIG;
-    float* ws2 = ws + 2 * BIG;
-    float* ws3 = ws + 3 * BIG;
-    float* lrbuf = ws + 4 * BIG;
-
-    unsigned short* wqThi = (unsigned short*)ws2;
-    unsigned short* wqTlo = wqThi + WIDTH * WIDTH;
-    unsigned short* wvThi = wqTlo + WIDTH * WIDTH;
-    unsigned short* wvTlo = wvThi + WIDTH * WIDTH;
-    unsigned short* wgThi = wvTlo + WIDTH * WIDTH;
-    unsigned short* wgTlo = wgThi + WIDTH * WIDTH;
-
-    unsigned short* Ahi = (unsigned short*)ws3;
-    unsigned short* Alo = Ahi + BIG;
-
-    unsigned short* XQhi = (unsigned short*)ws2;
+    float* xqk = ws;
+    float* XVb = ws + BIG;
+    unsigned short* XQhi = (unsigned short*)(ws + 2 * BIG);
     unsigned short* XQlo = XQhi + BIG;
-    unsigned short* XKhi = (unsigned short*)ws3;
+    unsigned short* XKhi = (unsigned short*)(ws + 3 * BIG);
     unsigned short* XKlo = XKhi + BIG;
-
-    unsigned short* woThi = (unsigned short*)ws1;
-    unsigned short* woTlo = woThi + WIDTH * WIDTH;
-    unsigned short* gzhi  = (unsigned short*)ws2;
-    unsigned short* gzlo  = gzhi + BIG;
-
-    float* xqk  = ws0;
-    float* XVb  = ws1;
+    float* tail = ws + 4 * BIG;
+    unsigned short* wThi  = (unsigned short*)tail;
+    unsigned short* wTlo  = wThi + (size_t)2304 * WIDTH;
+    unsigned short* woThi = wTlo + (size_t)2304 * WIDTH;
+    unsigned short* woTlo = woThi + (size_t)WIDTH * WIDTH;
+    float* lrbuf = (float*)(woTlo + (size_t)WIDTH * WIDTH);
+    unsigned short* gzhi = (unsigned short*)(ws + 2 * BIG);
+    unsigned short* gzlo = gzhi + BIG;
     float* gate = out;
-    float* ttto = ws0;
+    float* ttto = xqk;
 
     int M = BATCH * NSEQ;
-    dim3 gg(WIDTH / 128, M / 128);
-    dim3 wtg(WIDTH / 64, WIDTH / 64);
-
-    hsplit_kernel<<<(unsigned)(BIG / 1024), 256, 0, stream>>>(hidden, Ahi, Alo);
-    wtconv_kernel<<<wtg, 256, 0, stream>>>(wq, wqThi, wqTlo);
-    wtconv_kernel<<<wtg, 256, 0, stream>>>(wv, wvThi, wvTlo);
-    wtconv_kernel<<<wtg, 256, 0, stream>>>(wg, wgThi, wgTlo);
-    gemm_bf3<0><<<gg, 256, 0, stream>>>(Ahi, Alo, wqThi, wqTlo, xqk, M, WIDTH, WIDTH);
-    gemm_bf3<0><<<gg, 256, 0, stream>>>(Ahi, Alo, wvThi, wvTlo, XVb, M, WIDTH, WIDTH);
-    gemm_bf3<1><<<gg, 256, 0, stream>>>(Ahi, Alo, wgThi, wgTlo, gate, M, WIDTH, WIDTH);
+    wtconv3_kernel<<<dim3(12, 12, 3), 256, 0, stream>>>(wq, wv, wg, wThi, wTlo);
+    gemm_qv_kernel<<<dim3(12, M / 128), 256, 0, stream>>>(hidden, wThi, wTlo, xqk, XVb);
     conv_rope_kernel<<<M, 384, 0, stream>>>(xqk, ckq, cbq, ckk, cbk, XQhi, XQlo, XKhi, XKlo);
     lr_kernel<<<M / 4, 256, 0, stream>>>(hidden, lrk, lrb, lrbuf);
-    scan3_kernel<<<BATCH * HEADS, 256, 0, stream>>>(XQhi, XQlo, XKhi, XKlo, XVb, lrbuf,
-                                                    W1, b1, tns, tnb, lti, ttto);
-    wtconv_kernel<<<wtg, 256, 0, stream>>>(wo, woThi, woTlo);
+    mega_kernel<<<960, 256, 0, stream>>>(XQhi, XQlo, XKhi, XKlo, XVb, lrbuf,
+                                         W1, b1, tns, tnb, lti, ttto,
+                                         wo, woThi, woTlo,
+                                         hidden, wThi + (size_t)1536 * WIDTH,
+                                         wTlo + (size_t)1536 * WIDTH, gate);
     postgate_kernel<<<M, 256, 0, stream>>>(ttto, gate, pns, pnb, gzhi, gzlo);
-    gemm_bf3<0><<<gg, 256, 0, stream>>>(gzhi, gzlo, woThi, woTlo, out, M, WIDTH, WIDTH);
-}
+    gemm_out_kernel<<<dim3(6, M / 128), 256, 0, stream>>>(gzhi, gzlo, woThi, woTlo, out);
+}
```

Result: faster. 1.164 ms (-12.8%).
